# Kernel tuning notes

Measured on AMD Instinct MI355X. Metric: run time of the kernel, lower is better.

Reference implementation:

```python
import jax, jax.numpy as jnp
import numpy as np

D_MODEL, D_K, H = 1024, 64, 16
B, S = 2, 2048

def setup_inputs() -> dict:
    key = jax.random.key(0)
    ks = jax.random.split(key, 9)
    s_in = 1.0 / np.sqrt(D_MODEL)
    x = jax.random.normal(ks[0], (B, S, D_MODEL), dtype=jnp.float32)
    Wq = jax.random.uniform(ks[1], (H, D_MODEL, D_K), jnp.float32, -s_in, s_in)
    bq = jax.random.uniform(ks[2], (H, D_K), jnp.float32, -s_in, s_in)
    Wk = jax.random.uniform(ks[3], (H, D_MODEL, D_K), jnp.float32, -s_in, s_in)
    bk = jax.random.uniform(ks[4], (H, D_K), jnp.float32, -s_in, s_in)
    Wv = jax.random.uniform(ks[5], (H, D_MODEL, D_K), jnp.float32, -s_in, s_in)
    bv = jax.random.uniform(ks[6], (H, D_K), jnp.float32, -s_in, s_in)
    Wo = jax.random.uniform(ks[7], (D_MODEL, D_MODEL), jnp.float32, -s_in, s_in)
    bo = jax.random.uniform(ks[8], (D_MODEL,), jnp.float32, -s_in, s_in)
    return {"x": x, "Wq": Wq, "bq": bq, "Wk": Wk, "bk": bk,
            "Wv": Wv, "bv": bv, "Wo": Wo, "bo": bo}

def reference(x, Wq, bq, Wk, bk, Wv, bv, Wo, bo):
    # PositionLinear = Linear + ReLU (the ReLU is part of the original math)
    Q = jax.nn.relu(jnp.einsum('bsd,hdk->bhsk', x, Wq) + bq[:, None, :])
    K = jax.nn.relu(jnp.einsum('bsd,hdk->bhsk', x, Wk) + bk[:, None, :])
    V = jax.nn.relu(jnp.einsum('bsd,hdk->bhsk', x, Wv) + bv[:, None, :])
    scale = jnp.sqrt(jnp.float32(Q.shape[-1]))
    scores = jnp.einsum('bhsk,bhtk->bhst', Q, K) / scale  # [B,H,S,S]
    attn = jax.nn.softmax(scores, axis=-1)
    ctx = jnp.einsum('bhst,bhtk->bhsk', attn, V)
    # concat heads along feature dim (head order matches torch.cat(output, 2))
    ctx = jnp.transpose(ctx, (0, 2, 1, 3)).reshape(x.shape[0], x.shape[1], -1)
    out = jax.nn.relu(ctx @ Wo + bo)
    return out
```

## Files before the change

kernel.cpp:

```cpp
#include <hip/hip_runtime.h>
#include <cstddef>

#define D_MODEL 1024
#define DK 64
#define NH 16
#define NB 2
#define SEQ 2048

typedef __attribute__((ext_vector_type(8))) short bf16x8;
typedef __attribute__((ext_vector_type(4))) float floatx4;
typedef __attribute__((ext_vector_type(2))) unsigned uintx2;

static __device__ __forceinline__ unsigned short f2bf(float f) {
    union { float f; unsigned u; } v; v.f = f;
    unsigned r = (v.u + 0x7fffu + ((v.u >> 16) & 1u)) >> 16;
    return (unsigned short)r;
}

static __device__ __forceinline__ unsigned pk2bf(float lo, float hi) {
    unsigned ua = __float_as_uint(lo) + 0x8000u;
    unsigned ub = __float_as_uint(hi) + 0x8000u;
    return __builtin_amdgcn_perm(ub, ua, 0x07060302u);
}

static __device__ __forceinline__ float swz16(float x) {
    return __int_as_float(__builtin_amdgcn_ds_swizzle(__float_as_int(x), 0x401F));
}

static __device__ __forceinline__ void gld16(const unsigned short* g, unsigned short* l) {
    __builtin_amdgcn_global_load_lds(
        (const __attribute__((address_space(1))) unsigned int*)g,
        (__attribute__((address_space(3))) unsigned int*)l, 16, 0, 0);
}

__global__ __launch_bounds__(256) void convert_x(const float* __restrict__ x,
                                                 unsigned short* __restrict__ xb)
{
    const size_t i = ((size_t)blockIdx.x * 256 + threadIdx.x) * 16;
#pragma unroll
    for (int c = 0; c < 16; c += 4) {
        float4 v = *(const float4*)&x[i + c];
        uint2 pk;
        pk.x = (unsigned)f2bf(v.x) | ((unsigned)f2bf(v.y) << 16);
        pk.y = (unsigned)f2bf(v.z) | ((unsigned)f2bf(v.w) << 16);
        *(uint2*)&xb[i + c] = pk;
    }
}

__global__ __launch_bounds__(256) void pack_w(
    const float* __restrict__ Wq, const float* __restrict__ Wk,
    const float* __restrict__ Wv, const float* __restrict__ Wo,
    unsigned short* __restrict__ Bqkv, unsigned short* __restrict__ Bo)
{
    __shared__ float T[64][65];
    const int t   = blockIdx.x;
    const int tid = threadIdx.x;
    const int rr   = tid >> 2;
    const int cseg = (tid & 3) * 16;

    const float* src;
    unsigned short* dst;
    if (t < 768) {
        const int proj = t / 256, rem = t % 256;
        const int h = rem >> 4, d0 = (rem & 15) * 64;
        const float* W = proj == 0 ? Wq : (proj == 1 ? Wk : Wv);
        src = W + ((size_t)h * 1024 + d0) * 64;
#pragma unroll
        for (int c = 0; c < 16; c += 4) {
            float4 v = *(const float4*)&src[(size_t)rr * 64 + cseg + c];
            T[rr][cseg + c + 0] = v.x; T[rr][cseg + c + 1] = v.y;
            T[rr][cseg + c + 2] = v.z; T[rr][cseg + c + 3] = v.w;
        }
        __syncthreads();
        dst = &Bqkv[((size_t)proj * 1024 + h * 64 + rr) * 1024 + d0 + cseg];
    } else {
        const int t2 = t - 768;
        const int k0 = (t2 >> 4) * 64, nb0 = (t2 & 15) * 64;
#pragma unroll
        for (int c = 0; c < 16; c += 4) {
            float4 v = *(const float4*)&Wo[(size_t)(k0 + rr) * 1024 + nb0 + cseg + c];
            T[rr][cseg + c + 0] = v.x; T[rr][cseg + c + 1] = v.y;
            T[rr][cseg + c + 2] = v.z; T[rr][cseg + c + 3] = v.w;
        }
        __syncthreads();
        dst = &Bo[(size_t)(nb0 + rr) * 1024 + k0 + cseg];
    }
    unsigned int w[8];
#pragma unroll
    for (int ii = 0; ii < 8; ii++) {
        unsigned short lo = f2bf(T[cseg + ii * 2 + 0][rr]);
        unsigned short hi = f2bf(T[cseg + ii * 2 + 1][rr]);
        w[ii] = (unsigned)lo | ((unsigned)hi << 16);
    }
    *(uint4*)(dst + 0) = make_uint4(w[0], w[1], w[2], w[3]);
    *(uint4*)(dst + 8) = make_uint4(w[4], w[5], w[6], w[7]);
}

__global__ __launch_bounds__(256) void gemm_qkv(
    const unsigned short* __restrict__ Abf,
    const unsigned short* __restrict__ Bp,
    const float* __restrict__ bq, const float* __restrict__ bk,
    const float* __restrict__ bv,
    unsigned short* __restrict__ Qo, unsigned short* __restrict__ Ko,
    unsigned short* __restrict__ Vo)
{
    __shared__ __align__(16) unsigned short As[128 * 32];
    __shared__ __align__(16) unsigned short Bs[128 * 32];

    const int tid  = threadIdx.x;
    const int wv   = tid >> 6, lane = tid & 63;
    const int m0   = blockIdx.x * 128;
    const int n0   = blockIdx.y * 128;
    const int lq   = lane & 15, g = lane >> 4;
    const int wm   = (wv >> 1) * 64;
    const int wn   = (wv & 1) * 64;
    const int srow = lane >> 2;
    const int sseg = (lane & 3) * 8;

    floatx4 acc[4][4];
#pragma unroll
    for (int i = 0; i < 4; i++)
#pragma unroll
        for (int j = 0; j < 4; j++) acc[i][j] = (floatx4){0.f, 0.f, 0.f, 0.f};

    for (int k0 = 0; k0 < 1024; k0 += 32) {
#pragma unroll
        for (int r = 0; r < 2; r++) {
            const int chunk = wv * 2 + r;
            const int row   = chunk * 16 + srow;
            gld16(&Abf[(size_t)(m0 + row) * 1024 + k0 + sseg], &As[chunk * 512]);
            gld16(&Bp [(size_t)(n0 + row) * 1024 + k0 + sseg], &Bs[chunk * 512]);
        }
        __syncthreads();
        bf16x8 af[4], bfv[4];
#pragma unroll
        for (int i = 0; i < 4; i++)
            af[i] = *(const bf16x8*)&As[(wm + i * 16 + lq) * 32 + g * 8];
#pragma unroll
        for (int j = 0; j < 4; j++)
            bfv[j] = *(const bf16x8*)&Bs[(wn + j * 16 + lq) * 32 + g * 8];
#pragma unroll
        for (int i = 0; i < 4; i++)
#pragma unroll
            for (int j = 0; j < 4; j++)
                acc[i][j] = __builtin_amdgcn_mfma_f32_16x16x32_bf16(af[i], bfv[j], acc[i][j], 0, 0, 0);
        __syncthreads();
    }

    const int proj = n0 >> 10;
    const float* bias = proj == 0 ? bq : (proj == 1 ? bk : bv);
    unsigned short* OutQK = proj == 0 ? Qo : Ko;

#pragma unroll
    for (int j = 0; j < 4; j++) {
        const int n  = n0 + wn + j * 16 + lq;
        const int nn = n & 1023;
        const int h  = nn >> 6, dk = nn & 63;
        const float bb = bias[nn];
#pragma unroll
        for (int i = 0; i < 4; i++) {
            const int mbase = m0 + wm + i * 16 + g * 4;
            const int b_ = mbase >> 11;
            const int s_ = mbase & (SEQ - 1);
            const int bh = b_ * NH + h;
            if (proj < 2) {
                const size_t fb = (((size_t)bh * 128 + (s_ >> 4)) * 2 + (dk >> 5)) * 512
                                + (size_t)((((dk & 31) >> 3) * 16) + (s_ & 15)) * 8 + (dk & 7);
#pragma unroll
                for (int r = 0; r < 4; r++)
                    OutQK[fb + (size_t)r * 8] = f2bf(fmaxf(acc[i][j][r] + bb, 0.f));
            } else {
                const size_t fb = ((((size_t)bh * 32 + (s_ >> 6)) * 4 + (dk >> 4)) * 2
                                   + ((s_ >> 5) & 1)) * 512
                                + (size_t)((((s_ & 31) >> 3) * 16) + (dk & 15)) * 8 + (s_ & 7);
                uint2 pk;
                pk.x = (unsigned)f2bf(fmaxf(acc[i][j][0] + bb, 0.f))
                     | ((unsigned)f2bf(fmaxf(acc[i][j][1] + bb, 0.f)) << 16);
                pk.y = (unsigned)f2bf(fmaxf(acc[i][j][2] + bb, 0.f))
                     | ((unsigned)f2bf(fmaxf(acc[i][j][3] + bb, 0.f)) << 16);
                *(uint2*)&Vo[fb] = pk;
            }
        }
    }
}

__global__ __launch_bounds__(512, 4) void attn_kernel(
    const unsigned short* __restrict__ Qf,
    const unsigned short* __restrict__ Kf,
    const unsigned short* __restrict__ Vf,
    unsigned short* __restrict__ ctxb)
{
    __shared__ __align__(16) unsigned short KVs[2][16384];
    __shared__ float Lx[4][2][64];

    const int blk = blockIdx.x;
    const int xcd = blk & 7;
    const int j_  = blk >> 3;
    const int bh  = xcd * 4 + (j_ & 3);
    const int qt  = j_ >> 2;

    const int tid  = threadIdx.x;
    const int wv   = tid >> 6;
    const int lane = tid & 63;
    const int lq   = lane & 15;
    const int g    = lane >> 4;
    const int qq   = wv >> 1;
    const int kh   = wv & 1;

    const int q0 = qt * 128 + qq * 32;

    bf16x8 qa[2], qb[2];
    const size_t qfB = ((size_t)bh * 128 + (q0 >> 4)) * 1024 + (size_t)lane * 8;
#pragma unroll
    for (int t = 0; t < 2; t++) {
        qa[t] = *(const bf16x8*)&Qf[qfB + (size_t)t * 1024];
        qb[t] = *(const bf16x8*)&Qf[qfB + (size_t)t * 1024 + 512];
    }

    const float C  = 0.18033688011112042f;
    const float MC = 2.8853900817779267f;

    const unsigned short* KtB = &Kf[(size_t)bh * 131072];
    const unsigned short* VtB = &Vf[(size_t)bh * 131072];

    float l[2] = {0.f, 0.f};
    floatx4 acc[2][4];
#pragma unroll
    for (int t = 0; t < 2; t++)
#pragma unroll
        for (int n = 0; n < 4; n++) acc[t][n] = (floatx4){0.f, 0.f, 0.f, 0.f};

#pragma unroll
    for (int r = 0; r < 2; r++) {
        const int c = wv * 2 + r;
        gld16(&KtB[(size_t)c * 512 + lane * 8], &KVs[0][c * 512]);
        gld16(&VtB[(size_t)c * 512 + lane * 8], &KVs[0][8192 + c * 512]);
    }
    __syncthreads();

    for (int jt = 0; jt < SEQ / 128; jt++) {
        const int buf = jt & 1;

        const int jn = (jt + 1) & (SEQ / 128 - 1);
        const unsigned short* ktn = &KtB[(size_t)jn * 8192];
        const unsigned short* vtn = &VtB[(size_t)jn * 8192];
#pragma unroll
        for (int r = 0; r < 2; r++) {
            const int c = wv * 2 + r;
            gld16(&ktn[(size_t)c * 512 + lane * 8], &KVs[buf ^ 1][c * 512]);
            gld16(&vtn[(size_t)c * 512 + lane * 8], &KVs[buf ^ 1][8192 + c * 512]);
        }

        const unsigned short* kb = &KVs[buf][0];
        const unsigned short* vb = &KVs[buf][8192];

#pragma unroll
        for (int s = 0; s < 2; s++) {
            const int kg = 4 * kh + 2 * s;
            bf16x8 a0 = *(const bf16x8*)&kb[(kg + 0) * 1024 + lane * 8];
            bf16x8 a1 = *(const bf16x8*)&kb[(kg + 0) * 1024 + 512 + lane * 8];
            bf16x8 a2 = *(const bf16x8*)&kb[(kg + 1) * 1024 + lane * 8];
            bf16x8 a3 = *(const bf16x8*)&kb[(kg + 1) * 1024 + 512 + lane * 8];
            bf16x8 vr[4];
#pragma unroll
            for (int n = 0; n < 4; n++)
                vr[n] = *(const bf16x8*)&vb[(kh * 4 + n) * 1024 + s * 512 + lane * 8];

#pragma unroll
            for (int t = 0; t < 2; t++) {
                floatx4 s0 = (floatx4){0.f, 0.f, 0.f, 0.f};
                floatx4 s1 = (floatx4){0.f, 0.f, 0.f, 0.f};
                __builtin_amdgcn_s_setprio(1);
                s0 = __builtin_amdgcn_mfma_f32_16x16x32_bf16(a0, qa[t], s0, 0, 0, 0);
                s0 = __builtin_amdgcn_mfma_f32_16x16x32_bf16(a1, qb[t], s0, 0, 0, 0);
                s1 = __builtin_amdgcn_mfma_f32_16x16x32_bf16(a2, qa[t], s1, 0, 0, 0);
                s1 = __builtin_amdgcn_mfma_f32_16x16x32_bf16(a3, qb[t], s1, 0, 0, 0);
                __builtin_amdgcn_s_setprio(0);

                float p00 = __builtin_amdgcn_exp2f(fmaf(s0[0], C, -MC));
                float p01 = __builtin_amdgcn_exp2f(fmaf(s0[1], C, -MC));
                float p02 = __builtin_amdgcn_exp2f(fmaf(s0[2], C, -MC));
                float p03 = __builtin_amdgcn_exp2f(fmaf(s0[3], C, -MC));
                l[t] += (p00 + p01) + (p02 + p03);
                unsigned d0 = pk2bf(p00, p01);
                unsigned d1 = pk2bf(p02, p03);

                float p10 = __builtin_amdgcn_exp2f(fmaf(s1[0], C, -MC));
                float p11 = __builtin_amdgcn_exp2f(fmaf(s1[1], C, -MC));
                float p12 = __builtin_amdgcn_exp2f(fmaf(s1[2], C, -MC));
                float p13 = __builtin_amdgcn_exp2f(fmaf(s1[3], C, -MC));
                l[t] += (p10 + p11) + (p12 + p13);
                unsigned d2 = pk2bf(p10, p11);
                unsigned d3 = pk2bf(p12, p13);

                uintx2 r02 = __builtin_amdgcn_permlane32_swap(d0, d2, false, false);
                uintx2 r13 = __builtin_amdgcn_permlane32_swap(d1, d3, false, false);
                uintx2 f02 = __builtin_amdgcn_permlane16_swap(r02.x, r02.y, false, false);
                uintx2 f13 = __builtin_amdgcn_permlane16_swap(r13.x, r13.y, false, false);

                union { unsigned u[4]; bf16x8 v; } pbu;
                pbu.u[0] = f02.x;
                pbu.u[1] = f13.x;
                pbu.u[2] = f02.y;
                pbu.u[3] = f13.y;

                __builtin_amdgcn_s_setprio(1);
#pragma unroll
                for (int n = 0; n < 4; n++)
                    acc[t][n] = __builtin_amdgcn_mfma_f32_16x16x32_bf16(vr[n], pbu.v, acc[t][n], 0, 0, 0);
                __builtin_amdgcn_s_setprio(0);
            }
        }

        __syncthreads();
    }

#pragma unroll
    for (int t = 0; t < 2; t++) {
        l[t] += swz16(l[t]);
        l[t] += __shfl_xor(l[t], 32, 64);
    }

    float* red = (float*)&KVs[0][0] + (size_t)qq * 2048;
    if (kh == 1) {
#pragma unroll
        for (int t = 0; t < 2; t++) {
            Lx[qq][t][lane] = l[t];
#pragma unroll
            for (int n = 0; n < 4; n++)
                *(floatx4*)&red[(t * 4 + n) * 256 + lane * 4] = acc[t][n];
        }
    }
    __syncthreads();
    if (kh == 0) {
        const int b_ = bh >> 4, h_ = bh & 15;
#pragma unroll
        for (int t = 0; t < 2; t++) {
            const float lt = l[t] + Lx[qq][t][lane];
            const float li = 1.f / lt;
#pragma unroll
            for (int n = 0; n < 4; n++) {
                floatx4 a = acc[t][n];
                floatx4 b = *(const floatx4*)&red[(t * 4 + n) * 256 + lane * 4];
                uint2 pk;
                pk.x = pk2bf((a[0] + b[0]) * li, (a[1] + b[1]) * li);
                pk.y = pk2bf((a[2] + b[2]) * li, (a[3] + b[3]) * li);
                *(uint2*)&ctxb[((size_t)(b_ * SEQ) + q0 + t * 16 + lq) * D_MODEL
                               + h_ * DK + n * 16 + g * 4] = pk;
            }
        }
    }
}

__global__ __launch_bounds__(256) void gemm_o(
    const unsigned short* __restrict__ Abf,
    const unsigned short* __restrict__ Bp,
    const float* __restrict__ bo,
    float* __restrict__ out)
{
    __shared__ __align__(16) unsigned short As[64 * 32];
    __shared__ __align__(16) unsigned short Bs[64 * 32];

    const int tid  = threadIdx.x;
    const int wv   = tid >> 6, lane = tid & 63;
    const int bid  = blockIdx.x;
    const int swz  = (bid & 7) * 128 + (bid >> 3);
    const int m0   = (swz & 63) * 64;
    const int n0   = (swz >> 6) * 64;
    const int lq   = lane & 15, g = lane >> 4;
    const int wm   = (wv >> 1) * 32;
    const int wn   = (wv & 1) * 32;
    const int srow = lane >> 2;
    const int sseg = (lane & 3) * 8;

    floatx4 acc[2][2];
#pragma unroll
    for (int i = 0; i < 2; i++)
#pragma unroll
        for (int j = 0; j < 2; j++) acc[i][j] = (floatx4){0.f, 0.f, 0.f, 0.f};

    for (int k0 = 0; k0 < 1024; k0 += 32) {
        const int row = wv * 16 + srow;
        gld16(&Abf[(size_t)(m0 + row) * 1024 + k0 + sseg], &As[wv * 512]);
        gld16(&Bp [(size_t)(n0 + row) * 1024 + k0 + sseg], &Bs[wv * 512]);
        __syncthreads();
        bf16x8 af[2], bfv[2];
#pragma unroll
        for (int i = 0; i < 2; i++)
            af[i] = *(const bf16x8*)&As[(wm + i * 16 + lq) * 32 + g * 8];
#pragma unroll
        for (int j = 0; j < 2; j++)
            bfv[j] = *(const bf16x8*)&Bs[(wn + j * 16 + lq) * 32 + g * 8];
#pragma unroll
        for (int i = 0; i < 2; i++)
#pragma unroll
            for (int j = 0; j < 2; j++)
                acc[i][j] = __builtin_amdgcn_mfma_f32_16x16x32_bf16(af[i], bfv[j], acc[i][j], 0, 0, 0);
        __syncthreads();
    }

#pragma unroll
    for (int j = 0; j < 2; j++) {
        const int n  = n0 + wn + j * 16 + lq;
        const float bb = bo[n];
#pragma unroll
        for (int i = 0; i < 2; i++) {
#pragma unroll
            for (int r = 0; r < 4; r++) {
                const int m = m0 + wm + i * 16 + g * 4 + r;
                out[(size_t)m * 1024 + n] = fmaxf(acc[i][j][r] + bb, 0.f);
            }
        }
    }
}

extern "C" void kernel_launch(void* const* d_in, const int* in_sizes, int n_in,
                              void* d_out, int out_size, void* d_ws, size_t ws_size,
                              hipStream_t stream) {
    const float* x  = (const float*)d_in[0];
    const float* Wq = (const float*)d_in[1];
    const float* bq = (const float*)d_in[2];
    const float* Wk = (const float*)d_in[3];
    const float* bk = (const float*)d_in[4];
    const float* Wv = (const float*)d_in[5];
    const float* bv = (const float*)d_in[6];
    const float* Wo = (const float*)d_in[7];
    const float* bo = (const float*)d_in[8];
    float* out = (float*)d_out;

    const size_t perE = (size_t)NB * NH * SEQ * DK;
    unsigned short* xbf  = (unsigned short*)d_ws;
    unsigned short* Bqkv = xbf  + (size_t)4096 * 1024;
    unsigned short* Bo   = Bqkv + (size_t)3072 * 1024;
    unsigned short* Qfr  = Bo   + (size_t)1024 * 1024;
    unsigned short* Kfr  = Qfr + perE;
    unsigned short* Vfr  = Kfr + perE;
    unsigned short* Cbf  = Vfr + perE;

    convert_x<<<1024, 256, 0, stream>>>(x, xbf);
    pack_w<<<1024, 256, 0, stream>>>(Wq, Wk, Wv, Wo, Bqkv, Bo);
    gemm_qkv<<<dim3(32, 24), 256, 0, stream>>>(xbf, Bqkv, bq, bk, bv, Qfr, Kfr, Vfr);
    attn_kernel<<<512, 512, 0, stream>>>(Qfr, Kfr, Vfr, Cbf);
    gemm_o<<<1024, 256, 0, stream>>>(Cbf, Bo, bo, out);
}
```

Baseline: 193.2 us.

## Merge prep kernels, deepen QKV GEMM K-step, drop attention setprio

Merges the x conversion and weight packing into one launch, using block index ranges to pick the branch, which removes one kernel launch. The QKV GEMM now stages 64-wide K slices per barrier instead of 32, halving the number of syncs, and adds a launch-bounds occupancy hint of 3. The s_setprio bracketing around the MFMAs in the attention kernel is removed. The larger LDS tiles and the occupancy hint may reduce occupancy or add register pressure, and removing setprio changes how waves are scheduled.

```diff
diff --git a/kernel.cpp b/kernel.cpp
--- a/kernel.cpp
+++ b/kernel.cpp
@@ -33,28 +33,29 @@
         (__attribute__((address_space(3))) unsigned int*)l, 16, 0, 0);
 }
 
-__global__ __launch_bounds__(256) void convert_x(const float* __restrict__ x,
-                                                 unsigned short* __restrict__ xb)
-{
-    const size_t i = ((size_t)blockIdx.x * 256 + threadIdx.x) * 16;
-#pragma unroll
-    for (int c = 0; c < 16; c += 4) {
-        float4 v = *(const float4*)&x[i + c];
-        uint2 pk;
-        pk.x = (unsigned)f2bf(v.x) | ((unsigned)f2bf(v.y) << 16);
-        pk.y = (unsigned)f2bf(v.z) | ((unsigned)f2bf(v.w) << 16);
-        *(uint2*)&xb[i + c] = pk;
-    }
-}
-
-__global__ __launch_bounds__(256) void pack_w(
+__global__ __launch_bounds__(256) void prep(
+    const float* __restrict__ x, unsigned short* __restrict__ xb,
     const float* __restrict__ Wq, const float* __restrict__ Wk,
     const float* __restrict__ Wv, const float* __restrict__ Wo,
     unsigned short* __restrict__ Bqkv, unsigned short* __restrict__ Bo)
 {
     __shared__ float T[64][65];
-    const int t   = blockIdx.x;
     const int tid = threadIdx.x;
+
+    if (blockIdx.x < 1024) {
+        const size_t i = ((size_t)blockIdx.x * 256 + tid) * 16;
+#pragma unroll
+        for (int c = 0; c < 16; c += 4) {
+            float4 v = *(const float4*)&x[i + c];
+            uint2 pk;
+            pk.x = (unsigned)f2bf(v.x) | ((unsigned)f2bf(v.y) << 16);
+            pk.y = (unsigned)f2bf(v.z) | ((unsigned)f2bf(v.w) << 16);
+            *(uint2*)&xb[i + c] = pk;
+        }
+        return;
+    }
+
+    const int t   = blockIdx.x - 1024;
     const int rr   = tid >> 2;
     const int cseg = (tid & 3) * 16;
 
@@ -96,7 +97,7 @@
     *(uint4*)(dst + 8) = make_uint4(w[4], w[5], w[6], w[7]);
 }
 
-__global__ __launch_bounds__(256) void gemm_qkv(
+__global__ __launch_bounds__(256, 3) void gemm_qkv(
     const unsigned short* __restrict__ Abf,
     const unsigned short* __restrict__ Bp,
     const float* __restrict__ bq, const float* __restrict__ bk,
@@ -104,8 +105,8 @@
     unsigned short* __restrict__ Qo, unsigned short* __restrict__ Ko,
     unsigned short* __restrict__ Vo)
 {
-    __shared__ __align__(16) unsigned short As[128 * 32];
-    __shared__ __align__(16) unsigned short Bs[128 * 32];
+    __shared__ __align__(16) unsigned short As[128 * 64];
+    __shared__ __align__(16) unsigned short Bs[128 * 64];
 
     const int tid  = threadIdx.x;
     const int wv   = tid >> 6, lane = tid & 63;
@@ -123,27 +124,35 @@
 #pragma unroll
         for (int j = 0; j < 4; j++) acc[i][j] = (floatx4){0.f, 0.f, 0.f, 0.f};
 
-    for (int k0 = 0; k0 < 1024; k0 += 32) {
-#pragma unroll
-        for (int r = 0; r < 2; r++) {
-            const int chunk = wv * 2 + r;
-            const int row   = chunk * 16 + srow;
-            gld16(&Abf[(size_t)(m0 + row) * 1024 + k0 + sseg], &As[chunk * 512]);
-            gld16(&Bp [(size_t)(n0 + row) * 1024 + k0 + sseg], &Bs[chunk * 512]);
-        }
-        __syncthreads();
-        bf16x8 af[4], bfv[4];
-#pragma unroll
-        for (int i = 0; i < 4; i++)
-            af[i] = *(const bf16x8*)&As[(wm + i * 16 + lq) * 32 + g * 8];
-#pragma unroll
-        for (int j = 0; j < 4; j++)
-            bfv[j] = *(const bf16x8*)&Bs[(wn + j * 16 + lq) * 32 + g * 8];
-#pragma unroll
-        for (int i = 0; i < 4; i++)
+    for (int k0 = 0; k0 < 1024; k0 += 64) {
+#pragma unroll
+        for (int p = 0; p < 2; p++) {
+#pragma unroll
+            for (int r = 0; r < 2; r++) {
+                const int chunk = wv * 2 + r;
+                const int row   = chunk * 16 + srow;
+                gld16(&Abf[(size_t)(m0 + row) * 1024 + k0 + p * 32 + sseg],
+                      &As[p * 4096 + chunk * 512]);
+                gld16(&Bp [(size_t)(n0 + row) * 1024 + k0 + p * 32 + sseg],
+                      &Bs[p * 4096 + chunk * 512]);
+            }
+        }
+        __syncthreads();
+#pragma unroll
+        for (int p = 0; p < 2; p++) {
+            bf16x8 af[4], bfv[4];
+#pragma unroll
+            for (int i = 0; i < 4; i++)
+                af[i] = *(const bf16x8*)&As[p * 4096 + (wm + i * 16 + lq) * 32 + g * 8];
 #pragma unroll
             for (int j = 0; j < 4; j++)
-                acc[i][j] = __builtin_amdgcn_mfma_f32_16x16x32_bf16(af[i], bfv[j], acc[i][j], 0, 0, 0);
+                bfv[j] = *(const bf16x8*)&Bs[p * 4096 + (wn + j * 16 + lq) * 32 + g * 8];
+#pragma unroll
+            for (int i = 0; i < 4; i++)
+#pragma unroll
+                for (int j = 0; j < 4; j++)
+                    acc[i][j] = __builtin_amdgcn_mfma_f32_16x16x32_bf16(af[i], bfv[j], acc[i][j], 0, 0, 0);
+        }
         __syncthreads();
     }
 
@@ -270,12 +279,10 @@
             for (int t = 0; t < 2; t++) {
                 floatx4 s0 = (floatx4){0.f, 0.f, 0.f, 0.f};
                 floatx4 s1 = (floatx4){0.f, 0.f, 0.f, 0.f};
-                __builtin_amdgcn_s_setprio(1);
                 s0 = __builtin_amdgcn_mfma_f32_16x16x32_bf16(a0, qa[t], s0, 0, 0, 0);
                 s0 = __builtin_amdgcn_mfma_f32_16x16x32_bf16(a1, qb[t], s0, 0, 0, 0);
                 s1 = __builtin_amdgcn_mfma_f32_16x16x32_bf16(a2, qa[t], s1, 0, 0, 0);
                 s1 = __builtin_amdgcn_mfma_f32_16x16x32_bf16(a3, qb[t], s1, 0, 0, 0);
-                __builtin_amdgcn_s_setprio(0);
 
                 float p00 = __builtin_amdgcn_exp2f(fmaf(s0[0], C, -MC));
                 float p01 = __builtin_amdgcn_exp2f(fmaf(s0[1], C, -MC));
@@ -304,11 +311,9 @@
                 pbu.u[2] = f02.y;
                 pbu.u[3] = f13.y;
 
-                __builtin_amdgcn_s_setprio(1);
 #pragma unroll
                 for (int n = 0; n < 4; n++)
                     acc[t][n] = __builtin_amdgcn_mfma_f32_16x16x32_bf16(vr[n], pbu.v, acc[t][n], 0, 0, 0);
-                __builtin_amdgcn_s_setprio(0);
             }
         }
 
@@ -437,8 +442,7 @@
     unsigned short* Vfr  = Kfr + perE;
     unsigned short* Cbf  = Vfr + perE;
 
-    convert_x<<<1024, 256, 0, stream>>>(x, xbf);
-    pack_w<<<1024, 256, 0, stream>>>(Wq, Wk, Wv, Wo, Bqkv, Bo);
+    prep<<<2048, 256, 0, stream>>>(x, xbf, Wq, Wk, Wv, Wo, Bqkv, Bo);
     gemm_qkv<<<dim3(32, 24), 256, 0, stream>>>(xbf, Bqkv, bq, bk, bv, Qfr, Kfr, Vfr);
     attn_kernel<<<512, 512, 0, stream>>>(Qfr, Kfr, Vfr, Cbf);
     gemm_o<<<1024, 256, 0, stream>>>(Cbf, Bo, bo, out);
```

Measured after the change: 188.6 us. 1.02x faster.

## Merge prep kernels, compute softmax row sums via MFMA, drop setprio

Applied to the files above, without the earlier changes.

Merges the x-to-bf16 conversion and weight packing into one launch, saving a kernel launch and its gap. In the attention kernel, the softmax denominator is now an extra MFMA of the bf16 probabilities against a vector of ones, replacing per-lane fp32 adds and the final cross-lane swizzle and shuffle reductions. The s_setprio hints around the MFMA blocks are removed. The denominator now sums the bf16-rounded probabilities, which matches the numerator more closely, but adds one MFMA per tile to the matrix pipe.

```diff
diff --git a/kernel.cpp b/kernel.cpp
--- a/kernel.cpp
+++ b/kernel.cpp
@@ -23,38 +23,35 @@
     return __builtin_amdgcn_perm(ub, ua, 0x07060302u);
 }
 
-static __device__ __forceinline__ float swz16(float x) {
-    return __int_as_float(__builtin_amdgcn_ds_swizzle(__float_as_int(x), 0x401F));
-}
-
 static __device__ __forceinline__ void gld16(const unsigned short* g, unsigned short* l) {
     __builtin_amdgcn_global_load_lds(
         (const __attribute__((address_space(1))) unsigned int*)g,
         (__attribute__((address_space(3))) unsigned int*)l, 16, 0, 0);
 }
 
-__global__ __launch_bounds__(256) void convert_x(const float* __restrict__ x,
-                                                 unsigned short* __restrict__ xb)
-{
-    const size_t i = ((size_t)blockIdx.x * 256 + threadIdx.x) * 16;
-#pragma unroll
-    for (int c = 0; c < 16; c += 4) {
-        float4 v = *(const float4*)&x[i + c];
-        uint2 pk;
-        pk.x = (unsigned)f2bf(v.x) | ((unsigned)f2bf(v.y) << 16);
-        pk.y = (unsigned)f2bf(v.z) | ((unsigned)f2bf(v.w) << 16);
-        *(uint2*)&xb[i + c] = pk;
-    }
-}
-
-__global__ __launch_bounds__(256) void pack_w(
+__global__ __launch_bounds__(256) void prep(
+    const float* __restrict__ x, unsigned short* __restrict__ xb,
     const float* __restrict__ Wq, const float* __restrict__ Wk,
     const float* __restrict__ Wv, const float* __restrict__ Wo,
     unsigned short* __restrict__ Bqkv, unsigned short* __restrict__ Bo)
 {
     __shared__ float T[64][65];
-    const int t   = blockIdx.x;
     const int tid = threadIdx.x;
+
+    if (blockIdx.x < 1024) {
+        const size_t i = ((size_t)blockIdx.x * 256 + tid) * 16;
+#pragma unroll
+        for (int c = 0; c < 16; c += 4) {
+            float4 v = *(const float4*)&x[i + c];
+            uint2 pk;
+            pk.x = (unsigned)f2bf(v.x) | ((unsigned)f2bf(v.y) << 16);
+            pk.y = (unsigned)f2bf(v.z) | ((unsigned)f2bf(v.w) << 16);
+            *(uint2*)&xb[i + c] = pk;
+        }
+        return;
+    }
+
+    const int t   = blockIdx.x - 1024;
     const int rr   = tid >> 2;
     const int cseg = (tid & 3) * 16;
 
@@ -220,15 +217,21 @@
     const float C  = 0.18033688011112042f;
     const float MC = 2.8853900817779267f;
 
+    const short one_bf = (short)0x3F80;
+    const bf16x8 ones8 = (bf16x8){one_bf, one_bf, one_bf, one_bf,
+                                  one_bf, one_bf, one_bf, one_bf};
+
     const unsigned short* KtB = &Kf[(size_t)bh * 131072];
     const unsigned short* VtB = &Vf[(size_t)bh * 131072];
 
-    float l[2] = {0.f, 0.f};
+    floatx4 accl[2];
     floatx4 acc[2][4];
 #pragma unroll
-    for (int t = 0; t < 2; t++)
+    for (int t = 0; t < 2; t++) {
+        accl[t] = (floatx4){0.f, 0.f, 0.f, 0.f};
 #pragma unroll
         for (int n = 0; n < 4; n++) acc[t][n] = (floatx4){0.f, 0.f, 0.f, 0.f};
+    }
 
 #pragma unroll
     for (int r = 0; r < 2; r++) {
@@ -270,18 +273,15 @@
             for (int t = 0; t < 2; t++) {
                 floatx4 s0 = (floatx4){0.f, 0.f, 0.f, 0.f};
                 floatx4 s1 = (floatx4){0.f, 0.f, 0.f, 0.f};
-                __builtin_amdgcn_s_setprio(1);
                 s0 = __builtin_amdgcn_mfma_f32_16x16x32_bf16(a0, qa[t], s0, 0, 0, 0);
                 s0 = __builtin_amdgcn_mfma_f32_16x16x32_bf16(a1, qb[t], s0, 0, 0, 0);
                 s1 = __builtin_amdgcn_mfma_f32_16x16x32_bf16(a2, qa[t], s1, 0, 0, 0);
                 s1 = __builtin_amdgcn_mfma_f32_16x16x32_bf16(a3, qb[t], s1, 0, 0, 0);
-                __builtin_amdgcn_s_setprio(0);
 
                 float p00 = __builtin_amdgcn_exp2f(fmaf(s0[0], C, -MC));
                 float p01 = __builtin_amdgcn_exp2f(fmaf(s0[1], C, -MC));
                 float p02 = __builtin_amdgcn_exp2f(fmaf(s0[2], C, -MC));
                 float p03 = __builtin_amdgcn_exp2f(fmaf(s0[3], C, -MC));
-                l[t] += (p00 + p01) + (p02 + p03);
                 unsigned d0 = pk2bf(p00, p01);
                 unsigned d1 = pk2bf(p02, p03);
 
@@ -289,7 +289,6 @@
                 float p11 = __builtin_amdgcn_exp2f(fmaf(s1[1], C, -MC));
                 float p12 = __builtin_amdgcn_exp2f(fmaf(s1[2], C, -MC));
                 float p13 = __builtin_amdgcn_exp2f(fmaf(s1[3], C, -MC));
-                l[t] += (p10 + p11) + (p12 + p13);
                 unsigned d2 = pk2bf(p10, p11);
                 unsigned d3 = pk2bf(p12, p13);
 
@@ -304,28 +303,22 @@
                 pbu.u[2] = f02.y;
                 pbu.u[3] = f13.y;
 
-                __builtin_amdgcn_s_setprio(1);
+                accl[t] = __builtin_amdgcn_mfma_f32_16x16x32_bf16(ones8, pbu.v, accl[t], 0, 0, 0);
+
 #pragma unroll
                 for (int n = 0; n < 4; n++)
                     acc[t][n] = __builtin_amdgcn_mfma_f32_16x16x32_bf16(vr[n], pbu.v, acc[t][n], 0, 0, 0);
-                __builtin_amdgcn_s_setprio(0);
             }
         }
 
         __syncthreads();
-    }
-
-#pragma unroll
-    for (int t = 0; t < 2; t++) {
-        l[t] += swz16(l[t]);
-        l[t] += __shfl_xor(l[t], 32, 64);
     }
 
     float* red = (float*)&KVs[0][0] + (size_t)qq * 2048;
     if (kh == 1) {
 #pragma unroll
         for (int t = 0; t < 2; t++) {
-            Lx[qq][t][lane] = l[t];
+            Lx[qq][t][lane] = accl[t][0];
 #pragma unroll
             for (int n = 0; n < 4; n++)
                 *(floatx4*)&red[(t * 4 + n) * 256 + lane * 4] = acc[t][n];
@@ -336,7 +329,7 @@
         const int b_ = bh >> 4, h_ = bh & 15;
 #pragma unroll
         for (int t = 0; t < 2; t++) {
-            const float lt = l[t] + Lx[qq][t][lane];
+            const float lt = accl[t][0] + Lx[qq][t][lane];
             const float li = 1.f / lt;
 #pragma unroll
             for (int n = 0; n < 4; n++) {
@@ -437,8 +430,7 @@
     unsigned short* Vfr  = Kfr + perE;
     unsigned short* Cbf  = Vfr + perE;
 
-    convert_x<<<1024, 256, 0, stream>>>(x, xbf);
-    pack_w<<<1024, 256, 0, stream>>>(Wq, Wk, Wv, Wo, Bqkv, Bo);
+    prep<<<2048, 256, 0, stream>>>(x, xbf, Wq, Wk, Wv, Wo, Bqkv, Bo);
     gemm_qkv<<<dim3(32, 24), 256, 0, stream>>>(xbf, Bqkv, bq, bk, bv, Qfr, Kfr, Vfr);
     attn_kernel<<<512, 512, 0, stream>>>(Qfr, Kfr, Vfr, Cbf);
     gemm_o<<<1024, 256, 0, stream>>>(Cbf, Bo, bo, out);
```

After: 184.5 us. -4.5%, faster.
